# Optimization experiments

Hardware: AMD Instinct MI355X
Metric: run time of the kernel (lower is better)

## Reference

```python
import jax, jax.numpy as jnp
import numpy as np

H = 50  # LSTM units
T = 10  # NUMBARS
F = 5   # input features
B = 131072


def _lstm(x, W, U, b):
    """Keras-default LSTM. x: [B,T,Fin], W: [Fin,4H], U: [H,4H], b: [4H].
    Gate order i,f,g(c),o; sigmoid recurrent act, tanh cell act, zero init state.
    Returns (all_h [B,T,H], last_h [B,H])."""
    Bn = x.shape[0]
    h0 = jnp.zeros((Bn, H), x.dtype)
    c0 = jnp.zeros((Bn, H), x.dtype)

    def step(carry, xt):
        h, c = carry
        z = xt @ W + h @ U + b  # [B,4H]
        i, f, g, o = jnp.split(z, 4, axis=-1)
        i = jax.nn.sigmoid(i)
        f = jax.nn.sigmoid(f)
        g = jnp.tanh(g)
        o = jax.nn.sigmoid(o)
        c_new = f * c + i * g
        h_new = o * jnp.tanh(c_new)
        return (h_new, c_new), h_new

    (h_last, _), hs = jax.lax.scan(step, (h0, c0), jnp.swapaxes(x, 0, 1))
    return jnp.swapaxes(hs, 0, 1), h_last


def setup_inputs() -> dict:
    key = jax.random.key(0)
    ks = jax.random.split(key, 16)
    d = {"x": jax.random.normal(ks[0], (B, T, F), dtype=jnp.float32)}
    in_dims = [F, H, H, H]
    for l in range(4):
        s_in = 1.0 / np.sqrt(in_dims[l])
        s_h = 1.0 / np.sqrt(H)
        d[f"W{l+1}"] = jax.random.normal(ks[1 + 3 * l], (in_dims[l], 4 * H), dtype=jnp.float32) * s_in
        d[f"U{l+1}"] = jax.random.normal(ks[2 + 3 * l], (H, 4 * H), dtype=jnp.float32) * s_h
        # Keras unit_forget_bias: forget-gate bias = 1
        b = jnp.zeros((4 * H,), jnp.float32).at[H:2 * H].set(1.0)
        d[f"b{l+1}"] = b
    d["Wd1"] = jax.random.normal(ks[13], (H, 50), dtype=jnp.float32) * (1.0 / np.sqrt(H))
    d["bd1"] = jnp.zeros((50,), jnp.float32)
    d["Wd2"] = jax.random.normal(ks[14], (50, 1), dtype=jnp.float32) * (1.0 / np.sqrt(50))
    d["bd2"] = jnp.zeros((1,), jnp.float32)
    return d


def reference(x, W1, U1, b1, W2, U2, b2, W3, U3, b3, W4, U4, b4, Wd1, bd1, Wd2, bd2):
    # Dropout layers are identity at inference (Keras default training=False).
    h, _ = _lstm(x, W1, U1, b1)
    h, _ = _lstm(h, W2, U2, b2)
    h, _ = _lstm(h, W3, U3, b3)
    _, h = _lstm(h, W4, U4, b4)        # return_sequences=False -> last h [B,H]
    h = h @ Wd1 + bd1                   # Dense(50), linear activation
    out = jax.nn.sigmoid(h @ Wd2 + bd2) # Dense(1, sigmoid) -> [B,1]
    return out
```

## Files before the change

### kernel.cpp

```cpp
#include <hip/hip_runtime.h>


typedef __attribute__((ext_vector_type(8))) short short8;
typedef __attribute__((ext_vector_type(4))) float floatx4;
typedef __attribute__((ext_vector_type(2))) float float2v;
typedef unsigned short u16;
typedef unsigned int u32;

constexpr int H_ = 50, T_ = 10, F_ = 5;
constexpr int MTILE = 64;
constexpr int BLKT = 256;
constexpr float LOG2E = 1.4426950408889634f;

__device__ __forceinline__ float rcp_(float x) { return __builtin_amdgcn_rcpf(x); }
__device__ __forceinline__ float exp2_(float x) { return __builtin_amdgcn_exp2f(x); }
__device__ __forceinline__ float sig_nat(float x) {
  return rcp_(1.0f + exp2_(-LOG2E * x));
}

__device__ __forceinline__ u16 f2bf(float f) {
  union { float f; unsigned u; } v; v.f = f;
  unsigned r = v.u + 0x7FFFu + ((v.u >> 16) & 1u);
  return (u16)(r >> 16);
}
__device__ __forceinline__ float bf2f(u16 s) {
  union { unsigned u; float f; } v; v.u = ((unsigned)s) << 16;
  return v.f;
}
__device__ __forceinline__ unsigned pk_bf16(float a, float b) {
  return (unsigned)f2bf(a) | ((unsigned)f2bf(b) << 16);
}

__global__ void prep_kernel(
    const float* W1, const float* U1, const float* b1, const float* W2,
    const float* U2, const float* b2, const float* W3, const float* U3,
    const float* b3, const float* W4, const float* U4, const float* b4,
    const float* Wd1, const float* bd1, const float* Wd2, const float* bd2,
    u16* Wpp, float* biasP, float* vdense) {
  int idx = blockIdx.x * blockDim.x + threadIdx.x;
  const float* Wt[4] = {W1, W2, W3, W4};
  const float* Ut[4] = {U1, U2, U3, U4};
  const float* bt[4] = {b1, b2, b3, b4};
  const int fin[4] = {F_, H_, H_, H_};
  if (idx < 4 * 32768) {
    int l = idx >> 15, r = idx & 32767;
    int j = r & 7, lane = (r >> 3) & 63, w = (r >> 9) & 3, gI = (r >> 11) & 3,
        kt = r >> 13;
    int row = kt * 32 + (lane >> 4) * 8 + j;
    int u = w * 16 + (lane & 15);
    float val = 0.0f;
    if (u < H_) {
      if (row < 64) {
        if (row < fin[l]) val = Wt[l][row * 200 + gI * H_ + u];
      } else {
        int rr = row - 64;
        if (rr < H_) val = Ut[l][rr * 200 + gI * H_ + u];
      }
    }
    val *= (gI == 2) ? (2.0f * LOG2E) : (-LOG2E);
    Wpp[idx] = f2bf(val);
  } else if (idx < 4 * 32768 + 1024) {
    int r = idx - 4 * 32768;
    int l = r >> 8, q = r & 255, gI = q >> 6, u = q & 63;
    float val = (u < H_) ? bt[l][gI * H_ + u] : 0.0f;
    biasP[r] = val * ((gI == 2) ? (2.0f * LOG2E) : (-LOG2E));
  } else if (idx < 4 * 32768 + 1024 + 51) {
    int u = idx - (4 * 32768 + 1024);
    if (u < H_) {
      float s = 0.0f;
      for (int n = 0; n < H_; ++n) s += Wd1[u * H_ + n] * Wd2[n];
      vdense[u] = s;
    } else {
      float s = bd2[0];
      for (int n = 0; n < H_; ++n) s += bd1[n] * Wd2[n];
      vdense[50] = s;
    }
  }
}

template <bool FIRST, bool LAST>
__global__ __launch_bounds__(BLKT, 2) void lstm_mfma(
    const float* __restrict__ x0, u16* hbuf, const u16* __restrict__ Wpp,
    const float* __restrict__ biasP, int nblk, const float* __restrict__ vdense,
    float* __restrict__ out) {
  __shared__ __align__(16) u16 A[8192];
  const int tid = threadIdx.x;
  const int w = tid >> 6, lane = tid & 63;
  const int np = lane & 15, quad = lane >> 4;
  const int blk = blockIdx.x;
  const int b0 = blk * MTILE;
  const int u = w * 16 + np;

  short8 bfr[4][4];
#pragma unroll
  for (int kt = 0; kt < 4; ++kt)
#pragma unroll
    for (int gI = 0; gI < 4; ++gI)
      bfr[kt][gI] = *(const short8*)&Wpp[(((kt * 4 + gI) * 4 + w) * 64 + lane) * 8];

  float bv[4];
#pragma unroll
  for (int gI = 0; gI < 4; ++gI) bv[gI] = biasP[gI * 64 + u];

  for (int i = tid; i < 4096; i += BLKT) ((u32*)A)[i] = 0;

  float2v cst[8];
#pragma unroll
  for (int i = 0; i < 8; ++i) cst[i] = float2v{0.0f, 0.0f};

  short8 rx0, rx1;
  if constexpr (!FIRST) {
    const u16* s0 = hbuf + ((size_t)0 * nblk + blk) * 4096;
    rx0 = *(const short8*)(s0 + (size_t)tid * 8);
    rx1 = *(const short8*)(s0 + (size_t)(tid + 256) * 8);
  }

  const int kt_u = 2 + (w >> 1);
  const int cbase = ((kt_u * 4 + ((w & 1) * 2 + (np >> 3))) * 16 + quad * 4) * 8 + (np & 7);

  __syncthreads();

#pragma unroll 1
  for (int t = 0; t < T_; ++t) {
    if constexpr (!FIRST) {
      {
        int hc = tid, mt = hc >> 7, kk = (hc >> 6) & 1, rest = hc & 63;
        *(short8*)&A[((mt * 4 + kk) * 64 + rest) * 8] = rx0;
      }
      {
        int hc = tid + 256, mt = hc >> 7, kk = (hc >> 6) & 1, rest = hc & 63;
        *(short8*)&A[((mt * 4 + kk) * 64 + rest) * 8] = rx1;
      }
      if (t + 1 < T_) {
        const u16* s1 = hbuf + ((size_t)(t + 1) * nblk + blk) * 4096;
        rx0 = *(const short8*)(s1 + (size_t)tid * 8);
        rx1 = *(const short8*)(s1 + (size_t)(tid + 256) * 8);
      }
    } else {
      for (int e = tid; e < MTILE * F_; e += BLKT) {
        int row = e / F_, k = e - row * F_;
        int mt = row >> 4, rr = row & 15;
        A[(mt * 256 + rr) * 8 + k] =
            f2bf(x0[(size_t)(b0 + row) * (T_ * F_) + t * F_ + k]);
      }
    }
    __syncthreads();

    floatx4 acc[4][4];
#pragma unroll
    for (int mt = 0; mt < 4; ++mt)
#pragma unroll
      for (int gI = 0; gI < 4; ++gI)
        acc[mt][gI] = floatx4{bv[gI], bv[gI], bv[gI], bv[gI]};

#pragma unroll
    for (int kt = 0; kt < 4; ++kt) {
      if (FIRST && kt == 1) continue;
#pragma unroll
      for (int mt = 0; mt < 4; ++mt) {
        short8 af = *(const short8*)&A[(((mt * 4 + kt) * 4 + quad) * 16 + np) * 8];
#pragma unroll
        for (int gI = 0; gI < 4; ++gI)
          acc[mt][gI] = __builtin_amdgcn_mfma_f32_16x16x32_bf16(
              af, bfr[kt][gI], acc[mt][gI], 0, 0, 0);
      }
    }
    __syncthreads();

#pragma unroll
    for (int mt = 0; mt < 4; ++mt) {
#pragma unroll
      for (int p = 0; p < 2; ++p) {
        float2v di = {exp2_(acc[mt][0][2 * p]), exp2_(acc[mt][0][2 * p + 1])};
        float2v df = {exp2_(acc[mt][1][2 * p]), exp2_(acc[mt][1][2 * p + 1])};
        float2v dg = {exp2_(acc[mt][2][2 * p]), exp2_(acc[mt][2][2 * p + 1])};
        float2v do_ = {exp2_(acc[mt][3][2 * p]), exp2_(acc[mt][3][2 * p + 1])};
        di += 1.0f; df += 1.0f; dg += 1.0f; do_ += 1.0f;
        float2v m1 = di * df, m2 = do_ * dg;
        float2v P = m1 * m2;
        float Rs = rcp_(P.x * P.y);
        float2v R = {Rs * P.y, Rs * P.x};
        float2v i_ = (df * m2) * R;
        float2v f_ = (di * m2) * R;
        float2v o_ = (m1 * dg) * R;
        float2v g_ = 1.0f - 2.0f * ((m1 * do_) * R);
        float2v cn = f_ * cst[mt * 2 + p] + i_ * g_;
        cst[mt * 2 + p] = cn;
        float2v s = cn * (2.0f * LOG2E);
        float2v dc = {exp2_(s.x), exp2_(s.y)};
        dc += 1.0f;
        float Rc = rcp_(dc.x * dc.y);
        float2v tc = 1.0f - 2.0f * float2v{Rc * dc.y, Rc * dc.x};
        float2v h = o_ * tc;
        unsigned pk = pk_bf16(h.x, h.y);
        int a0 = cbase + mt * 2048 + (2 * p) * 8;
        A[a0] = (u16)pk;
        A[a0 + 8] = (u16)(pk >> 16);
      }
    }

    if constexpr (!LAST) {
      u16* dst = hbuf + ((size_t)t * nblk + blk) * 4096;
#pragma unroll
      for (int rep = 0; rep < 2; ++rep) {
        int e = lane + 64 * rep;
        int mt = e >> 5, rem = e & 31, qp = rem >> 4, rr = rem & 15;
        int quad_u = (w & 1) * 2 + qp;
        int ldsc = ((mt * 4 + kt_u) * 4 + quad_u) * 16 + rr;
        int hch = ((mt * 2 + (w >> 1)) * 4 + quad_u) * 16 + rr;
        *(short8*)&dst[(size_t)hch * 8] = *(const short8*)&A[ldsc * 8];
      }
    }
  }

  if constexpr (LAST) {
    __syncthreads();
    if (tid < MTILE) {
      int mt = tid >> 4, rr = tid & 15;
      float s = vdense[50];
      for (int k = 0; k < H_; ++k) {
        int ktu = 2 + (k >> 5), qd = (k & 31) >> 3, j = k & 7;
        s += bf2f(A[(((mt * 4 + ktu) * 4 + qd) * 16 + rr) * 8 + j]) * vdense[k];
      }
      out[b0 + tid] = sig_nat(s);
    }
  }
}

extern "C" void kernel_launch(void* const* d_in, const int* in_sizes, int n_in,
                              void* d_out, int out_size, void* d_ws,
                              size_t ws_size, hipStream_t stream) {
  const float* x = (const float*)d_in[0];
  const float* W1 = (const float*)d_in[1];
  const float* U1 = (const float*)d_in[2];
  const float* b1 = (const float*)d_in[3];
  const float* W2 = (const float*)d_in[4];
  const float* U2 = (const float*)d_in[5];
  const float* b2 = (const float*)d_in[6];
  const float* W3 = (const float*)d_in[7];
  const float* U3 = (const float*)d_in[8];
  const float* b3 = (const float*)d_in[9];
  const float* W4 = (const float*)d_in[10];
  const float* U4 = (const float*)d_in[11];
  const float* b4 = (const float*)d_in[12];
  const float* Wd1 = (const float*)d_in[13];
  const float* bd1 = (const float*)d_in[14];
  const float* Wd2 = (const float*)d_in[15];
  const float* bd2 = (const float*)d_in[16];

  const int Bn = in_sizes[0] / (T_ * F_);
  const int nblk = Bn / MTILE;
  char* ws = (char*)d_ws;
  u16* hbuf = (u16*)ws;
  size_t off = (size_t)T_ * nblk * 4096 * sizeof(u16);
  u16* Wpp = (u16*)(ws + off);
  float* biasP = (float*)(ws + off + 262144);
  float* vdense = (float*)(ws + off + 262144 + 4096);
  float* out = (float*)d_out;

  prep_kernel<<<(4 * 32768 + 1024 + 51 + 255) / 256, 256, 0, stream>>>(
      W1, U1, b1, W2, U2, b2, W3, U3, b3, W4, U4, b4, Wd1, bd1, Wd2, bd2, Wpp,
      biasP, vdense);

  dim3 grid(nblk), blkd(BLKT);
  lstm_mfma<true, false><<<grid, blkd, 0, stream>>>(
      x, hbuf, Wpp + 0 * 32768, biasP + 0 * 256, nblk, vdense, nullptr);
  lstm_mfma<false, false><<<grid, blkd, 0, stream>>>(
      nullptr, hbuf, Wpp + 1 * 32768, biasP + 1 * 256, nblk, vdense, nullptr);
  lstm_mfma<false, false><<<grid, blkd, 0, stream>>>(
      nullptr, hbuf, Wpp + 2 * 32768, biasP + 2 * 256, nblk, vdense, nullptr);
  lstm_mfma<false, true><<<grid, blkd, 0, stream>>>(
      nullptr, hbuf, Wpp + 3 * 32768, biasP + 3 * 256, nblk, vdense, out);
}
```

Baseline: 571.2 us.

## Raise occupancy by streaming weights from cache and moving cell state to LDS

Register-resident weight fragments are replaced by per-step global loads of the weight tiles, double-buffered across k-tiles, and the cell state moves from registers into a shared-memory buffer. Launch bounds go from 2 to 4 blocks per SM to use the freed registers. The next timestep's input is now fetched straight into LDS with global_load_lds after the MFMA phase, replacing the register prefetch. The cost is repeated weight traffic through cache every step, extra LDS use (which may cap occupancy anyway), and an added barrier per step.

Result: slower. 1.245 ms (+118.0%).

```diff
diff --git a/kernel.cpp b/kernel.cpp
--- a/kernel.cpp
+++ b/kernel.cpp
@@ -29,6 +29,12 @@
 }
 __device__ __forceinline__ unsigned pk_bf16(float a, float b) {
   return (unsigned)f2bf(a) | ((unsigned)f2bf(b) << 16);
+}
+
+__device__ __forceinline__ void gload_lds16(const u16* g, u16* l) {
+  __builtin_amdgcn_global_load_lds(
+      (const __attribute__((address_space(1))) u32*)g,
+      (__attribute__((address_space(3))) u32*)l, 16, 0, 0);
 }
 
 __global__ void prep_kernel(
@@ -79,11 +85,12 @@
 }
 
 template <bool FIRST, bool LAST>
-__global__ __launch_bounds__(BLKT, 2) void lstm_mfma(
-    const float* __restrict__ x0, u16* hbuf, const u16* __restrict__ Wpp,
+__global__ __launch_bounds__(BLKT, 4) void lstm_mfma(
+    const float* __restrict__ x0, u16* hbuf, const u16* Wpp,
     const float* __restrict__ biasP, int nblk, const float* __restrict__ vdense,
     float* __restrict__ out) {
   __shared__ __align__(16) u16 A[8192];
+  __shared__ __align__(16) float cbuf[4096];
   const int tid = threadIdx.x;
   const int w = tid >> 6, lane = tid & 63;
   const int np = lane & 15, quad = lane >> 4;
@@ -91,61 +98,52 @@
   const int b0 = blk * MTILE;
   const int u = w * 16 + np;
 
-  short8 bfr[4][4];
-#pragma unroll
-  for (int kt = 0; kt < 4; ++kt)
-#pragma unroll
-    for (int gI = 0; gI < 4; ++gI)
-      bfr[kt][gI] = *(const short8*)&Wpp[(((kt * 4 + gI) * 4 + w) * 64 + lane) * 8];
-
   float bv[4];
 #pragma unroll
   for (int gI = 0; gI < 4; ++gI) bv[gI] = biasP[gI * 64 + u];
 
-  for (int i = tid; i < 4096; i += BLKT) ((u32*)A)[i] = 0;
-
-  float2v cst[8];
-#pragma unroll
-  for (int i = 0; i < 8; ++i) cst[i] = float2v{0.0f, 0.0f};
-
-  short8 rx0, rx1;
-  if constexpr (!FIRST) {
-    const u16* s0 = hbuf + ((size_t)0 * nblk + blk) * 4096;
-    rx0 = *(const short8*)(s0 + (size_t)tid * 8);
-    rx1 = *(const short8*)(s0 + (size_t)(tid + 256) * 8);
-  }
-
+  floatx4* cld = (floatx4*)cbuf;
+#pragma unroll
+  for (int mt = 0; mt < 4; ++mt) cld[tid * 4 + mt] = floatx4{0, 0, 0, 0};
+
+  for (int i = tid; i < 2048; i += BLKT) {
+    int mt = i >> 9, r = i & 511;
+    ((u32*)A)[(mt * 256 + 128) * 4 + r] = 0;
+  }
+  if constexpr (FIRST) {
+    for (int i = tid; i < 2048; i += BLKT) {
+      int mt = i >> 9, r = i & 511;
+      ((u32*)A)[(mt * 256) * 4 + r] = 0;
+    }
+  }
+  __syncthreads();
+
+  const u16* wb = Wpp + w * 512 + lane * 8;
   const int kt_u = 2 + (w >> 1);
-  const int cbase = ((kt_u * 4 + ((w & 1) * 2 + (np >> 3))) * 16 + quad * 4) * 8 + (np & 7);
-
+  const int cbase =
+      ((kt_u * 4 + ((w & 1) * 2 + (np >> 3))) * 16 + quad * 4) * 8 + (np & 7);
+  constexpr int NKT = FIRST ? 3 : 4;
+  auto ktof = [](int i) { return FIRST ? ((i == 0) ? 0 : (i + 1)) : i; };
+
+  if constexpr (FIRST) {
+    for (int e = tid; e < MTILE * F_; e += BLKT) {
+      int row = e / F_, k = e - row * F_;
+      int mt = row >> 4, rr = row & 15;
+      A[(mt * 256 + rr) * 8 + k] = f2bf(x0[(size_t)(b0 + row) * (T_ * F_) + k]);
+    }
+  } else {
+    const u16* src = hbuf + (size_t)blk * 4096;
+#pragma unroll
+    for (int rep = 0; rep < 2; ++rep) {
+      int hcb = w * 64 + rep * 256;
+      int cb = ((hcb >> 7) * 4 + ((hcb >> 6) & 1)) * 64;
+      gload_lds16(src + (size_t)hcb * 8 + lane * 8, &A[cb * 8]);
+    }
+  }
   __syncthreads();
 
 #pragma unroll 1
   for (int t = 0; t < T_; ++t) {
-    if constexpr (!FIRST) {
-      {
-        int hc = tid, mt = hc >> 7, kk = (hc >> 6) & 1, rest = hc & 63;
-        *(short8*)&A[((mt * 4 + kk) * 64 + rest) * 8] = rx0;
-      }
-      {
-        int hc = tid + 256, mt = hc >> 7, kk = (hc >> 6) & 1, rest = hc & 63;
-        *(short8*)&A[((mt * 4 + kk) * 64 + rest) * 8] = rx1;
-      }
-      if (t + 1 < T_) {
-        const u16* s1 = hbuf + ((size_t)(t + 1) * nblk + blk) * 4096;
-        rx0 = *(const short8*)(s1 + (size_t)tid * 8);
-        rx1 = *(const short8*)(s1 + (size_t)(tid + 256) * 8);
-      }
-    } else {
-      for (int e = tid; e < MTILE * F_; e += BLKT) {
-        int row = e / F_, k = e - row * F_;
-        int mt = row >> 4, rr = row & 15;
-        A[(mt * 256 + rr) * 8 + k] =
-            f2bf(x0[(size_t)(b0 + row) * (T_ * F_) + t * F_ + k]);
-      }
-    }
-    __syncthreads();
-
     floatx4 acc[4][4];
 #pragma unroll
     for (int mt = 0; mt < 4; ++mt)
@@ -153,22 +151,53 @@
       for (int gI = 0; gI < 4; ++gI)
         acc[mt][gI] = floatx4{bv[gI], bv[gI], bv[gI], bv[gI]};
 
-#pragma unroll
-    for (int kt = 0; kt < 4; ++kt) {
-      if (FIRST && kt == 1) continue;
+    short8 bb[2][4];
+#pragma unroll
+    for (int gI = 0; gI < 4; ++gI)
+      bb[0][gI] = *(const volatile short8*)(wb + (ktof(0) * 4 + gI) * 2048);
+#pragma unroll
+    for (int ki = 0; ki < NKT; ++ki) {
+      const int kt = ktof(ki);
+      if (ki + 1 < NKT) {
+        const int ktn = ktof(ki + 1);
+#pragma unroll
+        for (int gI = 0; gI < 4; ++gI)
+          bb[(ki + 1) & 1][gI] =
+              *(const volatile short8*)(wb + (ktn * 4 + gI) * 2048);
+      }
 #pragma unroll
       for (int mt = 0; mt < 4; ++mt) {
         short8 af = *(const short8*)&A[(((mt * 4 + kt) * 4 + quad) * 16 + np) * 8];
 #pragma unroll
         for (int gI = 0; gI < 4; ++gI)
           acc[mt][gI] = __builtin_amdgcn_mfma_f32_16x16x32_bf16(
-              af, bfr[kt][gI], acc[mt][gI], 0, 0, 0);
+              af, bb[ki & 1][gI], acc[mt][gI], 0, 0, 0);
       }
     }
     __syncthreads();
 
+    if (t + 1 < T_) {
+      if constexpr (FIRST) {
+        for (int e = tid; e < MTILE * F_; e += BLKT) {
+          int row = e / F_, k = e - row * F_;
+          int mt = row >> 4, rr = row & 15;
+          A[(mt * 256 + rr) * 8 + k] =
+              f2bf(x0[(size_t)(b0 + row) * (T_ * F_) + (t + 1) * F_ + k]);
+        }
+      } else {
+        const u16* src = hbuf + ((size_t)(t + 1) * nblk + blk) * 4096;
+#pragma unroll
+        for (int rep = 0; rep < 2; ++rep) {
+          int hcb = w * 64 + rep * 256;
+          int cb = ((hcb >> 7) * 4 + ((hcb >> 6) & 1)) * 64;
+          gload_lds16(src + (size_t)hcb * 8 + lane * 8, &A[cb * 8]);
+        }
+      }
+    }
+
 #pragma unroll
     for (int mt = 0; mt < 4; ++mt) {
+      floatx4 cv = cld[tid * 4 + mt];
 #pragma unroll
       for (int p = 0; p < 2; ++p) {
         float2v di = {exp2_(acc[mt][0][2 * p]), exp2_(acc[mt][0][2 * p + 1])};
@@ -184,8 +213,10 @@
         float2v f_ = (di * m2) * R;
         float2v o_ = (m1 * dg) * R;
         float2v g_ = 1.0f - 2.0f * ((m1 * do_) * R);
-        float2v cn = f_ * cst[mt * 2 + p] + i_ * g_;
-        cst[mt * 2 + p] = cn;
+        float2v cp = {cv[2 * p], cv[2 * p + 1]};
+        float2v cn = f_ * cp + i_ * g_;
+        cv[2 * p] = cn.x;
+        cv[2 * p + 1] = cn.y;
         float2v s = cn * (2.0f * LOG2E);
         float2v dc = {exp2_(s.x), exp2_(s.y)};
         dc += 1.0f;
@@ -197,6 +228,7 @@
         A[a0] = (u16)pk;
         A[a0 + 8] = (u16)(pk >> 16);
       }
+      cld[tid * 4 + mt] = cv;
     }
 
     if constexpr (!LAST) {
@@ -211,10 +243,10 @@
         *(short8*)&dst[(size_t)hch * 8] = *(const short8*)&A[ldsc * 8];
       }
     }
+    __syncthreads();
   }
 
   if constexpr (LAST) {
-    __syncthreads();
     if (tid < MTILE) {
       int mt = tid >> 4, rr = tid & 15;
       float s = vdense[50];
```
